# Kernel optimization log

Measured on AMD Instinct MI355X. Metric: run time of the kernel, lower is better.

Reference implementation:

```python
import jax, jax.numpy as jnp
import numpy as np

N_NODES = 50000
N_EDGES = 800000
D = 128          # node_state_dim
H = 256          # edge hidden / message dim (= 2*D)
NH = 256         # node MLP hidden


def setup_inputs() -> dict:
    key = jax.random.key(0)
    ks = jax.random.split(key, 20)
    s = 0.05
    inp = {
        "node_states": jax.random.normal(ks[0], (N_NODES, D), jnp.float32),
        "edge_features": jax.random.normal(ks[1], (N_EDGES, 1), jnp.float32),
        "from_idx": jax.random.randint(ks[2], (N_EDGES,), 0, N_NODES, jnp.int32),
        "to_idx": jax.random.randint(ks[3], (N_EDGES,), 0, N_NODES, jnp.int32),
        # forward-direction message net: Linear(2D+1 -> H), ReLU, Linear(H -> H)
        "W1": jax.random.normal(ks[4], (2 * D + 1, H), jnp.float32) * s,
        "b1": jnp.zeros((H,), jnp.float32),
        "W2": jax.random.normal(ks[5], (H, H), jnp.float32) * s,
        "b2": jnp.zeros((H,), jnp.float32),
        # reverse-direction message net (separate params)
        "RW1": jax.random.normal(ks[6], (2 * D + 1, H), jnp.float32) * s,
        "Rb1": jnp.zeros((H,), jnp.float32),
        "RW2": jax.random.normal(ks[7], (H, H), jnp.float32) * s,
        "Rb2": jnp.zeros((H,), jnp.float32),
        # node update MLP: Linear(3D -> NH), ReLU, Linear(NH -> D)
        "Wn1": jax.random.normal(ks[8], (3 * D, NH), jnp.float32) * s,
        "bn1": jnp.zeros((NH,), jnp.float32),
        "Wn2": jax.random.normal(ks[9], (NH, D), jnp.float32) * s,
        "bn2": jnp.zeros((D,), jnp.float32),
    }
    return inp


def _mlp2(x, W1, b1, W2, b2):
    return jax.nn.relu(x @ W1 + b1) @ W2 + b2


def reference(node_states, edge_features, from_idx, to_idx,
              W1, b1, W2, b2, RW1, Rb1, RW2, Rb2, Wn1, bn1, Wn2, bn2):
    n_nodes = node_states.shape[0]
    from_states = node_states[from_idx]            # [E, D]
    to_states = node_states[to_idx]                # [E, D]

    # forward direction: messages go to to_idx
    edge_in = jnp.concatenate([from_states, to_states, edge_features], axis=-1)  # [E, 2D+1]
    msgs = _mlp2(edge_in, W1, b1, W2, b2)                                        # [E, H]
    agg = jax.ops.segment_sum(msgs, to_idx, num_segments=n_nodes)                # [N, H]

    # reverse direction: swap roles, aggregate onto from_idx
    redge_in = jnp.concatenate([to_states, from_states, edge_features], axis=-1)
    rmsgs = _mlp2(redge_in, RW1, Rb1, RW2, Rb2)
    agg = agg + jax.ops.segment_sum(rmsgs, from_idx, num_segments=n_nodes)

    # residual node update: MLP on [agg, node_states] -> [N, D]
    upd_in = jnp.concatenate([agg, node_states], axis=-1)                        # [N, 3D]
    return node_states + _mlp2(upd_in, Wn1, bn1, Wn2, bn2)
```

## Files before the change

### kernel.cpp

```cpp
#include <hip/hip_runtime.h>
#include <hip/hip_bf16.h>


typedef __bf16 bf16;
typedef __attribute__((ext_vector_type(8))) __bf16 bf16x8;
typedef __attribute__((ext_vector_type(4))) __bf16 bf16x4v;
typedef __attribute__((ext_vector_type(4))) float floatx4;
typedef __attribute__((ext_vector_type(2))) float floatx2;

#define DD 128
#define HH 256
#define CAPB 800
#define MAXBINS 3200

__device__ __forceinline__ bf16x8 ns8(const float* __restrict__ NS, int row, int col, int N) {
    bf16x8 v;
    if (row < N) {
        float4 f0 = *(const float4*)&NS[(size_t)row * DD + col];
        float4 f1 = *(const float4*)&NS[(size_t)row * DD + col + 4];
        v[0] = (bf16)f0.x; v[1] = (bf16)f0.y; v[2] = (bf16)f0.z; v[3] = (bf16)f0.w;
        v[4] = (bf16)f1.x; v[5] = (bf16)f1.y; v[6] = (bf16)f1.z; v[7] = (bf16)f1.w;
    } else {
        v = (bf16x8)(bf16)0.0f;
    }
    return v;
}

__global__ void k_pre(const float* __restrict__ W1, const float* __restrict__ RW1,
                      bf16* __restrict__ Wt1, int* __restrict__ gcur, int NBINS) {
    const int b = blockIdx.x, t = threadIdx.x;
    if (b < 512) {
        int idx = b * 256 + t;
        int n = idx >> 7, k = idx & 127;
        float v;
        if (n < 256)      v = W1[k * 256 + n];
        else if (n < 512) v = W1[(128 + k) * 256 + (n - 256)];
        else if (n < 768) v = RW1[k * 256 + (n - 512)];
        else              v = RW1[(128 + k) * 256 + (n - 768)];
        Wt1[idx] = (bf16)v;
    } else {
        int i = (b - 512) * 256 + t;
        if (i < NBINS) gcur[i] = 0;
    }
}

__global__ __launch_bounds__(256) void k_front(
    const float* __restrict__ NS, const int* __restrict__ from_idx,
    const int* __restrict__ to_idx, const float* __restrict__ ef,
    const float* __restrict__ W2, const float* __restrict__ RW2,
    const float* __restrict__ Wn1, const float* __restrict__ Wn2,
    const float* __restrict__ b2, const float* __restrict__ Rb2,
    const bf16* __restrict__ Wt1,
    int* __restrict__ gcur, int2* __restrict__ binbuf,
    unsigned char* __restrict__ Pn, bf16* __restrict__ Pf,
    bf16* __restrict__ Wth, bf16* __restrict__ Wt2,
    float* __restrict__ u, float* __restrict__ ru,
    int E, int N, int NP, int NBINS, int BINB, int MB) {
    __shared__ __align__(16) unsigned char smem[30720];
    const int b = blockIdx.x, t = threadIdx.x;

    if (b < BINB) {
        int* hist = (int*)smem;
        int* base = hist + MAXBINS;
        const int NBF = NP >> 5;
        for (int i = t; i < NBINS; i += 256) hist[i] = 0;
        __syncthreads();
        const int e0 = b * 2048;
        int f[8], tt[8]; float w[8]; bool valid[8];
#pragma unroll
        for (int q = 0; q < 8; ++q) {
            int e = e0 + q * 256 + t;
            valid[q] = e < E;
            int ec = valid[q] ? e : 0;
            f[q] = from_idx[ec]; tt[q] = to_idx[ec]; w[q] = ef[ec];
        }
#pragma unroll
        for (int q = 0; q < 8; ++q) {
            if (valid[q]) {
                atomicAdd(&hist[tt[q] >> 5], 1);
                atomicAdd(&hist[NBF + (f[q] >> 5)], 1);
            }
        }
        __syncthreads();
        for (int i = t; i < NBINS; i += 256) {
            int h = hist[i];
            base[i] = h ? atomicAdd(&gcur[i], h) : 0;
            hist[i] = 0;
        }
        __syncthreads();
#pragma unroll
        for (int q = 0; q < 8; ++q) {
            if (valid[q]) {
                int wb = __float_as_int(w[q]);
                int b1 = tt[q] >> 5;
                int r1 = base[b1] + atomicAdd(&hist[b1], 1);
                if (r1 < CAPB)
                    binbuf[(size_t)b1 * CAPB + r1] = make_int2(((tt[q] & 31) << 17) | f[q], wb);
                int b2i = NBF + (f[q] >> 5);
                int r2 = base[b2i] + atomicAdd(&hist[b2i], 1);
                if (r2 < CAPB)
                    binbuf[(size_t)b2i * CAPB + r2] = make_int2(((f[q] & 31) << 17) | tt[q], wb);
            }
        }
        return;
    }

    if (b < BINB + 769) {
        int bb = b - BINB;
        if (bb < 640) {
            int k = bb, m = t;
            float v;
            if (k < 512) {
                const float* Wsrc = (k < 256) ? W2 : RW2;
                int i = k & 255;
                float acc = 0.f;
                for (int j = 0; j < 256; ++j) acc += Wsrc[i * 256 + j] * Wn1[j * 256 + m];
                v = acc;
            } else {
                v = Wn1[(256 + k - 512) * 256 + m];
            }
            Wth[m * 640 + k] = (bf16)v;
        } else if (bb < 768) {
            int idx = (bb - 640) * 256 + t;
            int n = idx >> 8, k = idx & 255;
            Wt2[idx] = (bf16)Wn2[k * 128 + n];
        } else {
            int m = t;
            float a = 0.f, c2 = 0.f;
            for (int j = 0; j < 256; ++j) {
                float w = Wn1[j * 256 + m];
                a += b2[j] * w;
                c2 += Rb2[j] * w;
            }
            u[m] = a;
            ru[m] = c2;
        }
        return;
    }

    {
        bf16 (*As)[64][40] = (bf16(*)[64][40])smem;
        bf16 (*Bs)[2][64][40] = (bf16(*)[2][64][40])(smem + 10240);
        const int p = b - (BINB + 769);
        const int g = (p >> 6) * 8 + (p & 7);
        if (g >= MB) return;
        const int row0 = g * 64;
        const int colp = ((p >> 3) & 7) * 128;
        const int wv = t >> 6, lane = t & 63;
        const int l15 = lane & 15, quad = lane >> 4;
        const int srow = t >> 2, kc = (t & 3) * 8;
        floatx4 acc[2][4] = {};
        for (int k0 = 0; k0 < DD; k0 += 64) {
            bf16x8 av0 = ns8(NS, row0 + srow, k0 + kc, N);
            bf16x8 av1 = ns8(NS, row0 + srow, k0 + 32 + kc, N);
            bf16x8 bv00 = *(const bf16x8*)&Wt1[(size_t)(colp + srow) * DD + k0 + kc];
            bf16x8 bv01 = *(const bf16x8*)&Wt1[(size_t)(colp + srow) * DD + k0 + 32 + kc];
            bf16x8 bv10 = *(const bf16x8*)&Wt1[(size_t)(colp + 64 + srow) * DD + k0 + kc];
            bf16x8 bv11 = *(const bf16x8*)&Wt1[(size_t)(colp + 64 + srow) * DD + k0 + 32 + kc];
            __syncthreads();
            *(bf16x8*)&As[0][srow][kc] = av0;
            *(bf16x8*)&As[1][srow][kc] = av1;
            *(bf16x8*)&Bs[0][0][srow][kc] = bv00;
            *(bf16x8*)&Bs[0][1][srow][kc] = bv01;
            *(bf16x8*)&Bs[1][0][srow][kc] = bv10;
            *(bf16x8*)&Bs[1][1][srow][kc] = bv11;
            __syncthreads();
#pragma unroll
            for (int h = 0; h < 2; ++h) {
                bf16x8 afr[4];
#pragma unroll
                for (int r = 0; r < 4; ++r)
                    afr[r] = *(const bf16x8*)&As[h][r * 16 + l15][quad * 8];
#pragma unroll
                for (int cp = 0; cp < 2; ++cp) {
                    bf16x8 bfr = *(const bf16x8*)&Bs[cp][h][wv * 16 + l15][quad * 8];
#pragma unroll
                    for (int r = 0; r < 4; ++r)
                        acc[cp][r] = __builtin_amdgcn_mfma_f32_16x16x32_bf16(afr[r], bfr, acc[cp][r], 0, 0, 0);
                }
            }
        }
#pragma unroll
        for (int cp = 0; cp < 2; ++cp) {
            const int ocol = colp + cp * 64 + wv * 16 + l15;
            const int ch = ocol & 255;
            const int half = (ocol >> 9) & 1;
            const bool isNbr = ((ocol >> 8) & 1) == 0;
#pragma unroll
            for (int r = 0; r < 4; ++r)
#pragma unroll
                for (int i = 0; i < 4; ++i) {
                    int orow = row0 + r * 16 + quad * 4 + i;
                    float v = acc[cp][r][i];
                    if (isNbr) {
                        int pk = __builtin_amdgcn_cvt_pk_fp8_f32(v, v, 0, false);
                        Pn[(size_t)orow * 512 + half * 256 + ch] = (unsigned char)(pk & 0xFF);
                    } else {
                        Pf[(size_t)orow * 512 + half * 256 + ch] = (bf16)v;
                    }
                }
        }
    }
}

__global__ __launch_bounds__(256) void k_aggf(
    const unsigned char* __restrict__ Pn, const bf16* __restrict__ Pf,
    const int2* __restrict__ binbuf, const int* __restrict__ gcnt,
    const float* __restrict__ W1, const float* __restrict__ b1,
    const float* __restrict__ RW1, const float* __restrict__ Rb1,
    bf16* __restrict__ S_to, bf16* __restrict__ S_fr,
    int* __restrict__ deg, int NP) {
    __shared__ int hist[32], kstart[32], cur[32], scanbuf[32];
    __shared__ int2 srec[CAPB];
    const int b = blockIdx.x, t = threadIdx.x;
    const int NBF = NP >> 5;
    const bool rev = b >= NBF;
    const int node0 = (rev ? b - NBF : b) << 5;
    int cnt = gcnt[b]; if (cnt > CAPB) cnt = CAPB;
    const int2* bin = binbuf + (size_t)b * CAPB;
    if (t < 32) hist[t] = 0;
    __syncthreads();
    int2 h0 = make_int2(0, 0), h1 = h0, h2 = h0, h3 = h0;
    const bool p0 = t < cnt, p1 = t + 256 < cnt, p2 = t + 512 < cnt, p3 = t + 768 < cnt;
    if (p0) { h0 = bin[t];       atomicAdd(&hist[((unsigned)h0.x) >> 17], 1); }
    if (p1) { h1 = bin[t + 256]; atomicAdd(&hist[((unsigned)h1.x) >> 17], 1); }
    if (p2) { h2 = bin[t + 512]; atomicAdd(&hist[((unsigned)h2.x) >> 17], 1); }
    if (p3) { h3 = bin[t + 768]; atomicAdd(&hist[((unsigned)h3.x) >> 17], 1); }
    __syncthreads();
    if (t < 32) scanbuf[t] = hist[t];
    __syncthreads();
    for (int d = 1; d < 32; d <<= 1) {
        int v = (t < 32 && t >= d) ? scanbuf[t - d] : 0;
        __syncthreads();
        if (t < 32) scanbuf[t] += v;
        __syncthreads();
    }
    if (t < 32) { kstart[t] = scanbuf[t] - hist[t]; cur[t] = scanbuf[t] - hist[t]; }
    __syncthreads();
    if (p0) srec[atomicAdd(&cur[((unsigned)h0.x) >> 17], 1)] =
        make_int2((int)((((unsigned)h0.x) & 0x1FFFFu) << 9), h0.y);
    if (p1) srec[atomicAdd(&cur[((unsigned)h1.x) >> 17], 1)] =
        make_int2((int)((((unsigned)h1.x) & 0x1FFFFu) << 9), h1.y);
    if (p2) srec[atomicAdd(&cur[((unsigned)h2.x) >> 17], 1)] =
        make_int2((int)((((unsigned)h2.x) & 0x1FFFFu) << 9), h2.y);
    if (p3) srec[atomicAdd(&cur[((unsigned)h3.x) >> 17], 1)] =
        make_int2((int)((((unsigned)h3.x) & 0x1FFFFu) << 9), h3.y);
    __syncthreads();

    const int wv = t >> 6, lane = t & 63, c = lane * 4;
    const int fixoff = rev ? 256 : 0;
    const int coff = (rev ? 256 : 0) + c;
    const float* bb = rev ? Rb1 : b1;
    const float* wl = (rev ? RW1 : W1) + 65536;
    float4 bv = *(const float4*)&bb[c];
    float4 wv4 = *(const float4*)&wl[c];
    bf16* Sarr = rev ? S_fr : S_to;

    for (int key = wv; key < 32; key += 4) {
        const int node = node0 + key;
        bf16x4v pf = *(const bf16x4v*)&Pf[(size_t)node * 512 + fixoff + c];
        float fx0 = (float)pf[0] + bv.x;
        float fx1 = (float)pf[1] + bv.y;
        float fx2 = (float)pf[2] + bv.z;
        float fx3 = (float)pf[3] + bv.w;
        const int beg = kstart[key], kc2 = hist[key], end = beg + kc2;
        float e0 = 0.f, e1 = 0.f, e2 = 0.f, e3 = 0.f;
        float o0 = 0.f, o1 = 0.f, o2 = 0.f, o3 = 0.f;
        int j = beg;
        for (; j + 8 <= end; j += 8) {
            int2 rr[8]; int qq[8];
#pragma unroll
            for (int z = 0; z < 8; ++z) rr[z] = srec[j + z];
#pragma unroll
            for (int z = 0; z < 8; ++z)
                qq[z] = *(const int*)&Pn[(unsigned)rr[z].x + coff];
#pragma unroll
            for (int z = 0; z < 8; ++z) {
                float w = __int_as_float(rr[z].y);
                floatx2 lo = __builtin_amdgcn_cvt_pk_f32_fp8(qq[z], false);
                floatx2 hi = __builtin_amdgcn_cvt_pk_f32_fp8(qq[z], true);
                if (z & 1) {
                    o0 += fmaxf(__builtin_fmaf(w, wv4.x, fx0 + lo.x), 0.f);
                    o1 += fmaxf(__builtin_fmaf(w, wv4.y, fx1 + lo.y), 0.f);
                    o2 += fmaxf(__builtin_fmaf(w, wv4.z, fx2 + hi.x), 0.f);
                    o3 += fmaxf(__builtin_fmaf(w, wv4.w, fx3 + hi.y), 0.f);
                } else {
                    e0 += fmaxf(__builtin_fmaf(w, wv4.x, fx0 + lo.x), 0.f);
                    e1 += fmaxf(__builtin_fmaf(w, wv4.y, fx1 + lo.y), 0.f);
                    e2 += fmaxf(__builtin_fmaf(w, wv4.z, fx2 + hi.x), 0.f);
                    e3 += fmaxf(__builtin_fmaf(w, wv4.w, fx3 + hi.y), 0.f);
                }
            }
        }
        for (; j < end; ++j) {
            int2 r = srec[j];
            int q1 = *(const int*)&Pn[(unsigned)r.x + coff];
            float w = __int_as_float(r.y);
            floatx2 lo = __builtin_amdgcn_cvt_pk_f32_fp8(q1, false);
            floatx2 hi = __builtin_amdgcn_cvt_pk_f32_fp8(q1, true);
            e0 += fmaxf(__builtin_fmaf(w, wv4.x, fx0 + lo.x), 0.f);
            e1 += fmaxf(__builtin_fmaf(w, wv4.y, fx1 + lo.y), 0.f);
            e2 += fmaxf(__builtin_fmaf(w, wv4.z, fx2 + hi.x), 0.f);
            e3 += fmaxf(__builtin_fmaf(w, wv4.w, fx3 + hi.y), 0.f);
        }
        float a0 = e0 + o0, a1 = e1 + o1, a2 = e2 + o2, a3 = e3 + o3;
        bf16x4v o;
        o[0] = (bf16)a0; o[1] = (bf16)a1; o[2] = (bf16)a2; o[3] = (bf16)a3;
        *(bf16x4v*)&Sarr[(size_t)node * 256 + c] = o;
        if (lane == 0) deg[(rev ? NP : 0) + node] = kc2;
    }
}

__global__ __launch_bounds__(256) void k_node(
    const bf16* __restrict__ S_to, const bf16* __restrict__ S_fr,
    const float* __restrict__ NS, const bf16* __restrict__ Wth,
    const bf16* __restrict__ Wt2,
    const float* __restrict__ u, const float* __restrict__ ru,
    const float* __restrict__ bn1, const float* __restrict__ bn2,
    const int* __restrict__ deg, float* __restrict__ out, int NP, int N) {
    __shared__ __align__(16) unsigned char smem[33792];
    bf16 (*As)[40]  = (bf16(*)[40])smem;
    bf16 (*Bs)[40]  = (bf16(*)[40])(smem + 5120);
    bf16 (*Hs)[264] = (bf16(*)[264])smem;
    const int tid = threadIdx.x;
    const int wv = tid >> 6, lane = tid & 63;
    const int l15 = lane & 15, quad = lane >> 4;
    const int row0 = blockIdx.x * 64;
    const int srow = tid >> 2, kc = (tid & 3) * 8;
    floatx4 acc[4][4] = {};
    const int arow = row0 + srow;
    for (int k0 = 0; k0 < 640; k0 += 32) {
        bf16x8 av;
        if (k0 < 512) {
            const bf16* S = (k0 < 256) ? S_to : S_fr;
            av = *(const bf16x8*)&S[(size_t)arow * 256 + (k0 & 255) + kc];
        } else {
            av = ns8(NS, arow, (k0 - 512) + kc, N);
        }
        bf16x8 bv[4];
#pragma unroll
        for (int j = 0; j < 4; ++j)
            bv[j] = *(const bf16x8*)&Wth[(size_t)(srow + 64 * j) * 640 + k0 + kc];
        __syncthreads();
        *(bf16x8*)&As[srow][kc] = av;
#pragma unroll
        for (int j = 0; j < 4; ++j)
            *(bf16x8*)&Bs[srow + 64 * j][kc] = bv[j];
        __syncthreads();
#pragma unroll
        for (int s = 0; s < 4; ++s) {
            bf16x8 bfr = *(const bf16x8*)&Bs[wv * 64 + s * 16 + l15][quad * 8];
#pragma unroll
            for (int r = 0; r < 4; ++r) {
                bf16x8 afr = *(const bf16x8*)&As[r * 16 + l15][quad * 8];
                acc[s][r] = __builtin_amdgcn_mfma_f32_16x16x32_bf16(afr, bfr, acc[s][r], 0, 0, 0);
            }
        }
    }
    __syncthreads();
#pragma unroll
    for (int s = 0; s < 4; ++s) {
        int col = wv * 64 + s * 16 + l15;
        float uc = u[col], rc = ru[col], bc = bn1[col];
#pragma unroll
        for (int r = 0; r < 4; ++r)
#pragma unroll
            for (int i = 0; i < 4; ++i) {
                int row = r * 16 + quad * 4 + i;
                float v = acc[s][r][i] + (float)deg[row0 + row] * uc
                        + (float)deg[NP + row0 + row] * rc + bc;
                Hs[row][col] = (bf16)fmaxf(v, 0.f);
            }
    }
    __syncthreads();
    floatx4 acc2[2][4] = {};
    for (int k0 = 0; k0 < HH; k0 += 32) {
        bf16x8 afr[4];
#pragma unroll
        for (int r = 0; r < 4; ++r)
            afr[r] = *(const bf16x8*)&Hs[r * 16 + l15][k0 + quad * 8];
#pragma unroll
        for (int s = 0; s < 2; ++s) {
            int col = wv * 32 + s * 16 + l15;
            bf16x8 bfr = *(const bf16x8*)&Wt2[(size_t)col * HH + k0 + quad * 8];
#pragma unroll
            for (int r = 0; r < 4; ++r)
                acc2[s][r] = __builtin_amdgcn_mfma_f32_16x16x32_bf16(afr[r], bfr, acc2[s][r], 0, 0, 0);
        }
    }
#pragma unroll
    for (int s = 0; s < 2; ++s) {
        int ocol = wv * 32 + s * 16 + l15;
        float bb = bn2[ocol];
#pragma unroll
        for (int r = 0; r < 4; ++r)
#pragma unroll
            for (int i = 0; i < 4; ++i) {
                int orow = row0 + r * 16 + quad * 4 + i;
                if (orow < N)
                    out[(size_t)orow * DD + ocol] = acc2[s][r][i] + bb + NS[(size_t)orow * DD + ocol];
            }
    }
}

extern "C" void kernel_launch(void* const* d_in, const int* in_sizes, int n_in,
                              void* d_out, int out_size, void* d_ws, size_t ws_size,
                              hipStream_t stream) {
    const float* NS   = (const float*)d_in[0];
    const float* ef   = (const float*)d_in[1];
    const int* from_idx = (const int*)d_in[2];
    const int* to_idx   = (const int*)d_in[3];
    const float* W1  = (const float*)d_in[4];
    const float* b1  = (const float*)d_in[5];
    const float* W2  = (const float*)d_in[6];
    const float* b2  = (const float*)d_in[7];
    const float* RW1 = (const float*)d_in[8];
    const float* Rb1 = (const float*)d_in[9];
    const float* RW2 = (const float*)d_in[10];
    const float* Rb2 = (const float*)d_in[11];
    const float* Wn1 = (const float*)d_in[12];
    const float* bn1 = (const float*)d_in[13];
    const float* Wn2 = (const float*)d_in[14];
    const float* bn2 = (const float*)d_in[15];

    const int N  = in_sizes[0] / DD;
    const int E  = in_sizes[2];
    const int NP = ((N + 63) / 64) * 64;
    const int MB = NP / 64;
    const int NBF = NP / 32;
    const int NBINS = 2 * NBF;
    const int BINB = (E + 2047) / 2048;
    const int FRONT = BINB + 769 + 64 * ((MB + 7) / 8);
    const int PREB = 512 + (NBINS + 255) / 256;

    char* base = (char*)d_ws;
    size_t off_b = 0;
    auto alloc = [&](size_t b) { size_t o = off_b; off_b += (b + 255) & ~(size_t)255; return o; };
    unsigned char* Pn = (unsigned char*)(base + alloc((size_t)NP * 512));
    bf16* Pf   = (bf16*)(base + alloc((size_t)NP * 512 * 2));
    bf16* S_to = (bf16*)(base + alloc((size_t)NP * 256 * 2));
    bf16* S_fr = (bf16*)(base + alloc((size_t)NP * 256 * 2));
    int* deg   = (int*)(base + alloc((size_t)2 * NP * 4));
    int* gcur  = (int*)(base + alloc((size_t)NBINS * 4));
    int2* binbuf = (int2*)(base + alloc((size_t)NBINS * CAPB * 8));
    bf16* Wt1 = (bf16*)(base + alloc(1024 * 128 * 2));
    bf16* Wth = (bf16*)(base + alloc(256 * 640 * 2));
    bf16* Wt2 = (bf16*)(base + alloc(128 * 256 * 2));
    float* u  = (float*)(base + alloc(256 * 4));
    float* ru = (float*)(base + alloc(256 * 4));

    k_pre<<<PREB, 256, 0, stream>>>(W1, RW1, Wt1, gcur, NBINS);
    k_front<<<FRONT, 256, 0, stream>>>(NS, from_idx, to_idx, ef,
                                       W2, RW2, Wn1, Wn2, b2, Rb2, Wt1,
                                       gcur, binbuf, Pn, Pf, Wth, Wt2, u, ru,
                                       E, N, NP, NBINS, BINB, MB);
    k_aggf<<<NBINS, 256, 0, stream>>>(Pn, Pf, binbuf, gcur, W1, b1, RW1, Rb1,
                                      S_to, S_fr, deg, NP);
    k_node<<<MB, 256, 0, stream>>>(S_to, S_fr, NS, Wth, Wt2, u, ru, bn1, bn2,
                                   deg, (float*)d_out, NP, N);
}
```

Before: 311.1 us.

## Make node-projection GEMM persistent with register-resident weights and prefetched A tiles

The projection GEMM section previously launched one block per 64-row tile and 128-column panel, reloading weight tiles through shared memory each time. It now launches a fixed 512 blocks (8 panels x 64 blocks), each keeping its 128-column weight slice in registers and looping over row tiles with stride 64. The next tile's node states are prefetched into registers while MFMAs run. This removes redundant weight loads and shared-memory B staging, and cuts block count, at the cost of more registers and less parallelism if too few blocks fill the GPU.

```diff
diff --git a/kernel.cpp b/kernel.cpp
--- a/kernel.cpp
+++ b/kernel.cpp
@@ -140,65 +140,73 @@
 
     {
         bf16 (*As)[64][40] = (bf16(*)[64][40])smem;
-        bf16 (*Bs)[2][64][40] = (bf16(*)[2][64][40])(smem + 10240);
         const int p = b - (BINB + 769);
-        const int g = (p >> 6) * 8 + (p & 7);
-        if (g >= MB) return;
-        const int row0 = g * 64;
-        const int colp = ((p >> 3) & 7) * 128;
+        const int panel = p >> 6;
+        const int gstart = p & 63;
+        const int colp = panel * 128;
         const int wv = t >> 6, lane = t & 63;
         const int l15 = lane & 15, quad = lane >> 4;
         const int srow = t >> 2, kc = (t & 3) * 8;
-        floatx4 acc[2][4] = {};
-        for (int k0 = 0; k0 < DD; k0 += 64) {
-            bf16x8 av0 = ns8(NS, row0 + srow, k0 + kc, N);
-            bf16x8 av1 = ns8(NS, row0 + srow, k0 + 32 + kc, N);
-            bf16x8 bv00 = *(const bf16x8*)&Wt1[(size_t)(colp + srow) * DD + k0 + kc];
-            bf16x8 bv01 = *(const bf16x8*)&Wt1[(size_t)(colp + srow) * DD + k0 + 32 + kc];
-            bf16x8 bv10 = *(const bf16x8*)&Wt1[(size_t)(colp + 64 + srow) * DD + k0 + kc];
-            bf16x8 bv11 = *(const bf16x8*)&Wt1[(size_t)(colp + 64 + srow) * DD + k0 + 32 + kc];
+        bf16x8 breg[2][4];
+#pragma unroll
+        for (int cp = 0; cp < 2; ++cp)
+#pragma unroll
+            for (int h = 0; h < 4; ++h)
+                breg[cp][h] = *(const bf16x8*)&Wt1[(size_t)(colp + cp * 64 + wv * 16 + l15) * DD + h * 32 + quad * 8];
+        int g = gstart;
+        bf16x8 av[4];
+        if (g < MB) {
+#pragma unroll
+            for (int h = 0; h < 4; ++h)
+                av[h] = ns8(NS, g * 64 + srow, h * 32 + kc, N);
+        }
+        while (g < MB) {
+            const int row0 = g * 64;
             __syncthreads();
-            *(bf16x8*)&As[0][srow][kc] = av0;
-            *(bf16x8*)&As[1][srow][kc] = av1;
-            *(bf16x8*)&Bs[0][0][srow][kc] = bv00;
-            *(bf16x8*)&Bs[0][1][srow][kc] = bv01;
-            *(bf16x8*)&Bs[1][0][srow][kc] = bv10;
-            *(bf16x8*)&Bs[1][1][srow][kc] = bv11;
+#pragma unroll
+            for (int h = 0; h < 4; ++h)
+                *(bf16x8*)&As[h][srow][kc] = av[h];
             __syncthreads();
-#pragma unroll
-            for (int h = 0; h < 2; ++h) {
+            const int gn = g + 64;
+            if (gn < MB) {
+#pragma unroll
+                for (int h = 0; h < 4; ++h)
+                    av[h] = ns8(NS, gn * 64 + srow, h * 32 + kc, N);
+            }
+            floatx4 acc[2][4] = {};
+#pragma unroll
+            for (int h = 0; h < 4; ++h) {
                 bf16x8 afr[4];
 #pragma unroll
                 for (int r = 0; r < 4; ++r)
                     afr[r] = *(const bf16x8*)&As[h][r * 16 + l15][quad * 8];
 #pragma unroll
-                for (int cp = 0; cp < 2; ++cp) {
-                    bf16x8 bfr = *(const bf16x8*)&Bs[cp][h][wv * 16 + l15][quad * 8];
+                for (int cp = 0; cp < 2; ++cp)
 #pragma unroll
                     for (int r = 0; r < 4; ++r)
-                        acc[cp][r] = __builtin_amdgcn_mfma_f32_16x16x32_bf16(afr[r], bfr, acc[cp][r], 0, 0, 0);
-                }
-            }
-        }
-#pragma unroll
-        for (int cp = 0; cp < 2; ++cp) {
-            const int ocol = colp + cp * 64 + wv * 16 + l15;
-            const int ch = ocol & 255;
-            const int half = (ocol >> 9) & 1;
-            const bool isNbr = ((ocol >> 8) & 1) == 0;
-#pragma unroll
-            for (int r = 0; r < 4; ++r)
-#pragma unroll
-                for (int i = 0; i < 4; ++i) {
-                    int orow = row0 + r * 16 + quad * 4 + i;
-                    float v = acc[cp][r][i];
-                    if (isNbr) {
-                        int pk = __builtin_amdgcn_cvt_pk_fp8_f32(v, v, 0, false);
-                        Pn[(size_t)orow * 512 + half * 256 + ch] = (unsigned char)(pk & 0xFF);
-                    } else {
-                        Pf[(size_t)orow * 512 + half * 256 + ch] = (bf16)v;
+                        acc[cp][r] = __builtin_amdgcn_mfma_f32_16x16x32_bf16(afr[r], breg[cp][h], acc[cp][r], 0, 0, 0);
+            }
+#pragma unroll
+            for (int cp = 0; cp < 2; ++cp) {
+                const int ocol = colp + cp * 64 + wv * 16 + l15;
+                const int ch = ocol & 255;
+                const int half = (ocol >> 9) & 1;
+                const bool isNbr = ((ocol >> 8) & 1) == 0;
+#pragma unroll
+                for (int r = 0; r < 4; ++r)
+#pragma unroll
+                    for (int i = 0; i < 4; ++i) {
+                        int orow = row0 + r * 16 + quad * 4 + i;
+                        float v = acc[cp][r][i];
+                        if (isNbr) {
+                            int pk = __builtin_amdgcn_cvt_pk_fp8_f32(v, v, 0, false);
+                            Pn[(size_t)orow * 512 + half * 256 + ch] = (unsigned char)(pk & 0xFF);
+                        } else {
+                            Pf[(size_t)orow * 512 + half * 256 + ch] = (bf16)v;
+                        }
                     }
-                }
+            }
+            g = gn;
         }
     }
 }
@@ -430,7 +438,7 @@
     const int NBF = NP / 32;
     const int NBINS = 2 * NBF;
     const int BINB = (E + 2047) / 2048;
-    const int FRONT = BINB + 769 + 64 * ((MB + 7) / 8);
+    const int FRONT = BINB + 769 + 512;
     const int PREB = 512 + (NBINS + 255) / 256;
 
     char* base = (char*)d_ws;
```

New measurement: 325.8 us. 1.05x slower.

## Replace per-32-node bins with per-node fixed-capacity adjacency slots

Applied to the files above, without the earlier changes.

Edge binning now atomically increments a per-node degree counter in global memory and writes each record straight into a 64-slot per-node buffer. This removes the shared-memory histogram, global base reservation and the in-block counting sort in the aggregation kernel. Aggregation blocks now read their records directly from global memory, one wave per four nodes. In exchange there are two global atomics per edge on random addresses, and any edges beyond 64 per node are silently dropped. The degree counts stored for the node kernel now come straight from the counters and can exceed 64.

```diff
diff --git a/kernel.cpp b/kernel.cpp
--- a/kernel.cpp
+++ b/kernel.cpp
@@ -10,8 +10,7 @@
 
 #define DD 128
 #define HH 256
-#define CAPB 800
-#define MAXBINS 3200
+#define CAPN 64
 
 __device__ __forceinline__ bf16x8 ns8(const float* __restrict__ NS, int row, int col, int N) {
     bf16x8 v;
@@ -27,7 +26,7 @@
 }
 
 __global__ void k_pre(const float* __restrict__ W1, const float* __restrict__ RW1,
-                      bf16* __restrict__ Wt1, int* __restrict__ gcur, int NBINS) {
+                      bf16* __restrict__ Wt1, int* __restrict__ deg, int nzn) {
     const int b = blockIdx.x, t = threadIdx.x;
     if (b < 512) {
         int idx = b * 256 + t;
@@ -40,7 +39,7 @@
         Wt1[idx] = (bf16)v;
     } else {
         int i = (b - 512) * 256 + t;
-        if (i < NBINS) gcur[i] = 0;
+        if (i < nzn) deg[i] = 0;
     }
 }
 
@@ -51,20 +50,15 @@
     const float* __restrict__ Wn1, const float* __restrict__ Wn2,
     const float* __restrict__ b2, const float* __restrict__ Rb2,
     const bf16* __restrict__ Wt1,
-    int* __restrict__ gcur, int2* __restrict__ binbuf,
+    int* __restrict__ deg, int2* __restrict__ binbuf,
     unsigned char* __restrict__ Pn, bf16* __restrict__ Pf,
     bf16* __restrict__ Wth, bf16* __restrict__ Wt2,
     float* __restrict__ u, float* __restrict__ ru,
-    int E, int N, int NP, int NBINS, int BINB, int MB) {
+    int E, int N, int NP, int BINB, int MB) {
     __shared__ __align__(16) unsigned char smem[30720];
     const int b = blockIdx.x, t = threadIdx.x;
 
     if (b < BINB) {
-        int* hist = (int*)smem;
-        int* base = hist + MAXBINS;
-        const int NBF = NP >> 5;
-        for (int i = t; i < NBINS; i += 256) hist[i] = 0;
-        __syncthreads();
         const int e0 = b * 2048;
         int f[8], tt[8]; float w[8]; bool valid[8];
 #pragma unroll
@@ -77,29 +71,13 @@
 #pragma unroll
         for (int q = 0; q < 8; ++q) {
             if (valid[q]) {
-                atomicAdd(&hist[tt[q] >> 5], 1);
-                atomicAdd(&hist[NBF + (f[q] >> 5)], 1);
-            }
-        }
-        __syncthreads();
-        for (int i = t; i < NBINS; i += 256) {
-            int h = hist[i];
-            base[i] = h ? atomicAdd(&gcur[i], h) : 0;
-            hist[i] = 0;
-        }
-        __syncthreads();
-#pragma unroll
-        for (int q = 0; q < 8; ++q) {
-            if (valid[q]) {
                 int wb = __float_as_int(w[q]);
-                int b1 = tt[q] >> 5;
-                int r1 = base[b1] + atomicAdd(&hist[b1], 1);
-                if (r1 < CAPB)
-                    binbuf[(size_t)b1 * CAPB + r1] = make_int2(((tt[q] & 31) << 17) | f[q], wb);
-                int b2i = NBF + (f[q] >> 5);
-                int r2 = base[b2i] + atomicAdd(&hist[b2i], 1);
-                if (r2 < CAPB)
-                    binbuf[(size_t)b2i * CAPB + r2] = make_int2(((f[q] & 31) << 17) | tt[q], wb);
+                int s1 = atomicAdd(&deg[tt[q]], 1);
+                if (s1 < CAPN)
+                    binbuf[((size_t)tt[q] << 6) + s1] = make_int2(f[q] << 9, wb);
+                int s2 = atomicAdd(&deg[NP + f[q]], 1);
+                if (s2 < CAPN)
+                    binbuf[((size_t)(NP + f[q]) << 6) + s2] = make_int2(tt[q] << 9, wb);
             }
         }
         return;
@@ -205,49 +183,14 @@
 
 __global__ __launch_bounds__(256) void k_aggf(
     const unsigned char* __restrict__ Pn, const bf16* __restrict__ Pf,
-    const int2* __restrict__ binbuf, const int* __restrict__ gcnt,
+    const int2* __restrict__ binbuf, const int* __restrict__ deg,
     const float* __restrict__ W1, const float* __restrict__ b1,
     const float* __restrict__ RW1, const float* __restrict__ Rb1,
-    bf16* __restrict__ S_to, bf16* __restrict__ S_fr,
-    int* __restrict__ deg, int NP) {
-    __shared__ int hist[32], kstart[32], cur[32], scanbuf[32];
-    __shared__ int2 srec[CAPB];
-    const int b = blockIdx.x, t = threadIdx.x;
-    const int NBF = NP >> 5;
-    const bool rev = b >= NBF;
-    const int node0 = (rev ? b - NBF : b) << 5;
-    int cnt = gcnt[b]; if (cnt > CAPB) cnt = CAPB;
-    const int2* bin = binbuf + (size_t)b * CAPB;
-    if (t < 32) hist[t] = 0;
-    __syncthreads();
-    int2 h0 = make_int2(0, 0), h1 = h0, h2 = h0, h3 = h0;
-    const bool p0 = t < cnt, p1 = t + 256 < cnt, p2 = t + 512 < cnt, p3 = t + 768 < cnt;
-    if (p0) { h0 = bin[t];       atomicAdd(&hist[((unsigned)h0.x) >> 17], 1); }
-    if (p1) { h1 = bin[t + 256]; atomicAdd(&hist[((unsigned)h1.x) >> 17], 1); }
-    if (p2) { h2 = bin[t + 512]; atomicAdd(&hist[((unsigned)h2.x) >> 17], 1); }
-    if (p3) { h3 = bin[t + 768]; atomicAdd(&hist[((unsigned)h3.x) >> 17], 1); }
-    __syncthreads();
-    if (t < 32) scanbuf[t] = hist[t];
-    __syncthreads();
-    for (int d = 1; d < 32; d <<= 1) {
-        int v = (t < 32 && t >= d) ? scanbuf[t - d] : 0;
-        __syncthreads();
-        if (t < 32) scanbuf[t] += v;
-        __syncthreads();
-    }
-    if (t < 32) { kstart[t] = scanbuf[t] - hist[t]; cur[t] = scanbuf[t] - hist[t]; }
-    __syncthreads();
-    if (p0) srec[atomicAdd(&cur[((unsigned)h0.x) >> 17], 1)] =
-        make_int2((int)((((unsigned)h0.x) & 0x1FFFFu) << 9), h0.y);
-    if (p1) srec[atomicAdd(&cur[((unsigned)h1.x) >> 17], 1)] =
-        make_int2((int)((((unsigned)h1.x) & 0x1FFFFu) << 9), h1.y);
-    if (p2) srec[atomicAdd(&cur[((unsigned)h2.x) >> 17], 1)] =
-        make_int2((int)((((unsigned)h2.x) & 0x1FFFFu) << 9), h2.y);
-    if (p3) srec[atomicAdd(&cur[((unsigned)h3.x) >> 17], 1)] =
-        make_int2((int)((((unsigned)h3.x) & 0x1FFFFu) << 9), h3.y);
-    __syncthreads();
-
+    bf16* __restrict__ S_to, bf16* __restrict__ S_fr, int NP) {
+    const int t = threadIdx.x;
     const int wv = t >> 6, lane = t & 63, c = lane * 4;
+    const int g0 = blockIdx.x * 16 + wv * 4;
+    const bool rev = g0 >= NP;
     const int fixoff = rev ? 256 : 0;
     const int coff = (rev ? 256 : 0) + c;
     const float* bb = rev ? Rb1 : b1;
@@ -256,21 +199,25 @@
     float4 wv4 = *(const float4*)&wl[c];
     bf16* Sarr = rev ? S_fr : S_to;
 
-    for (int key = wv; key < 32; key += 4) {
-        const int node = node0 + key;
+#pragma unroll
+    for (int kk = 0; kk < 4; ++kk) {
+        const int g = g0 + kk;
+        const int node = rev ? g - NP : g;
+        int cnt = deg[g]; if (cnt > CAPN) cnt = CAPN;
+        cnt = __builtin_amdgcn_readfirstlane(cnt);
+        const int2* recs = binbuf + ((size_t)g << 6);
         bf16x4v pf = *(const bf16x4v*)&Pf[(size_t)node * 512 + fixoff + c];
         float fx0 = (float)pf[0] + bv.x;
         float fx1 = (float)pf[1] + bv.y;
         float fx2 = (float)pf[2] + bv.z;
         float fx3 = (float)pf[3] + bv.w;
-        const int beg = kstart[key], kc2 = hist[key], end = beg + kc2;
         float e0 = 0.f, e1 = 0.f, e2 = 0.f, e3 = 0.f;
         float o0 = 0.f, o1 = 0.f, o2 = 0.f, o3 = 0.f;
-        int j = beg;
-        for (; j + 8 <= end; j += 8) {
+        int j = 0;
+        for (; j + 8 <= cnt; j += 8) {
             int2 rr[8]; int qq[8];
 #pragma unroll
-            for (int z = 0; z < 8; ++z) rr[z] = srec[j + z];
+            for (int z = 0; z < 8; ++z) rr[z] = recs[j + z];
 #pragma unroll
             for (int z = 0; z < 8; ++z)
                 qq[z] = *(const int*)&Pn[(unsigned)rr[z].x + coff];
@@ -292,8 +239,8 @@
                 }
             }
         }
-        for (; j < end; ++j) {
-            int2 r = srec[j];
+        for (; j < cnt; ++j) {
+            int2 r = recs[j];
             int q1 = *(const int*)&Pn[(unsigned)r.x + coff];
             float w = __int_as_float(r.y);
             floatx2 lo = __builtin_amdgcn_cvt_pk_f32_fp8(q1, false);
@@ -307,7 +254,6 @@
         bf16x4v o;
         o[0] = (bf16)a0; o[1] = (bf16)a1; o[2] = (bf16)a2; o[3] = (bf16)a3;
         *(bf16x4v*)&Sarr[(size_t)node * 256 + c] = o;
-        if (lane == 0) deg[(rev ? NP : 0) + node] = kc2;
     }
 }
 
@@ -427,11 +373,10 @@
     const int E  = in_sizes[2];
     const int NP = ((N + 63) / 64) * 64;
     const int MB = NP / 64;
-    const int NBF = NP / 32;
-    const int NBINS = 2 * NBF;
     const int BINB = (E + 2047) / 2048;
     const int FRONT = BINB + 769 + 64 * ((MB + 7) / 8);
-    const int PREB = 512 + (NBINS + 255) / 256;
+    const int PREB = 512 + (2 * NP + 255) / 256;
+    const int AGGB = (2 * NP) / 16;
 
     char* base = (char*)d_ws;
     size_t off_b = 0;
@@ -441,21 +386,20 @@
     bf16* S_to = (bf16*)(base + alloc((size_t)NP * 256 * 2));
     bf16* S_fr = (bf16*)(base + alloc((size_t)NP * 256 * 2));
     int* deg   = (int*)(base + alloc((size_t)2 * NP * 4));
-    int* gcur  = (int*)(base + alloc((size_t)NBINS * 4));
-    int2* binbuf = (int2*)(base + alloc((size_t)NBINS * CAPB * 8));
+    int2* binbuf = (int2*)(base + alloc((size_t)2 * NP * CAPN * 8));
     bf16* Wt1 = (bf16*)(base + alloc(1024 * 128 * 2));
     bf16* Wth = (bf16*)(base + alloc(256 * 640 * 2));
     bf16* Wt2 = (bf16*)(base + alloc(128 * 256 * 2));
     float* u  = (float*)(base + alloc(256 * 4));
     float* ru = (float*)(base + alloc(256 * 4));
 
-    k_pre<<<PREB, 256, 0, stream>>>(W1, RW1, Wt1, gcur, NBINS);
+    k_pre<<<PREB, 256, 0, stream>>>(W1, RW1, Wt1, deg, 2 * NP);
     k_front<<<FRONT, 256, 0, stream>>>(NS, from_idx, to_idx, ef,
                                        W2, RW2, Wn1, Wn2, b2, Rb2, Wt1,
-                                       gcur, binbuf, Pn, Pf, Wth, Wt2, u, ru,
-                                       E, N, NP, NBINS, BINB, MB);
-    k_aggf<<<NBINS, 256, 0, stream>>>(Pn, Pf, binbuf, gcur, W1, b1, RW1, Rb1,
-                                      S_to, S_fr, deg, NP);
+                                       deg, binbuf, Pn, Pf, Wth, Wt2, u, ru,
+                                       E, N, NP, BINB, MB);
+    k_aggf<<<AGGB, 256, 0, stream>>>(Pn, Pf, binbuf, deg, W1, b1, RW1, Rb1,
+                                     S_to, S_fr, NP);
     k_node<<<MB, 256, 0, stream>>>(S_to, S_fr, NS, Wth, Wt2, u, ru, bn1, bn2,
                                    deg, (float*)d_out, NP, N);
 }
```

New measurement: 455.2 us. 1.46x slower.
